# Kernel optimization log

Measured on AMD Instinct MI355X. Metric: run time of the kernel, lower is better.

## Reference

```python
import jax, jax.numpy as jnp
import numpy as np

N = 20000      # nodes
E = 640000     # edges (avg degree 32)
F = 128        # hidden_channels == num_filters
RBF = 64       # num_rbf
H = 8          # num_heads
DH = F // H    # head dim
T = 5          # number of distinct element types present in z
CUT = 5.0      # cutoff_upper (cutoff_lower = 0)


def setup_inputs() -> dict:
    key = jax.random.key(0)
    ks = jax.random.split(key, 20)
    s = 0.05
    inp = {
        "x": jax.random.normal(ks[0], (N, F), jnp.float32),
        "z": jax.random.randint(ks[1], (N,), 0, T, jnp.int32),
        "edge_index": jax.random.randint(ks[2], (2, E), 0, N, jnp.int32),
        "edge_weight": jax.random.uniform(ks[3], (E,), jnp.float32) * CUT,
        "edge_attr": jax.random.normal(ks[4], (E, RBF), jnp.float32),
        # ElemConv params
        "lin1_w": jax.random.normal(ks[5], (F, F), jnp.float32) / np.sqrt(F),
        "f_w1": jax.random.normal(ks[6], (F, RBF), jnp.float32) / np.sqrt(RBF),
        "f_b1": jnp.zeros((F,), jnp.float32),
        "f_w2": jax.random.normal(ks[7], (F, F), jnp.float32) / np.sqrt(F),
        "f_b2": jnp.zeros((F,), jnp.float32),
        # ElemAttn params
        "q_w": jax.random.normal(ks[8], (F, F), jnp.float32) / np.sqrt(F),
        "q_b": jax.random.normal(ks[9], (F,), jnp.float32) * s,
        "k_w": jax.random.normal(ks[10], (F, F), jnp.float32) / np.sqrt(F),
        "k_b": jax.random.normal(ks[11], (F,), jnp.float32) * s,
        "v_w": jax.random.normal(ks[12], (F, F), jnp.float32) / np.sqrt(F),
        "v_b": jax.random.normal(ks[13], (F,), jnp.float32) * s,
        "o1_w": jax.random.normal(ks[14], (F, F), jnp.float32) / np.sqrt(F),
        "o1_b": jax.random.normal(ks[15], (F,), jnp.float32) * s,
        "o2_w": jax.random.normal(ks[16], (F, F), jnp.float32) / np.sqrt(F),
        "o2_b": jax.random.normal(ks[17], (F,), jnp.float32) * s,
    }
    return inp


def reference(x, z, edge_index, edge_weight, edge_attr,
              lin1_w, f_w1, f_b1, f_w2, f_b2,
              q_w, q_b, k_w, k_b, v_w, v_b, o1_w, o1_b, o2_w, o2_b):
    silu = jax.nn.silu
    src, dst = edge_index[0], edge_index[1]

    # ---- ElemConv ----
    # CosineCutoff (cutoff_lower = 0)
    C = 0.5 * (jnp.cos(edge_weight * (jnp.pi / CUT)) + 1.0)
    C = C * (edge_weight < CUT).astype(x.dtype)
    # filter_net(edge_attr) * C
    W = silu(edge_attr @ f_w1.T + f_b1) @ f_w2.T + f_b2          # [E, F]
    W = W * C[:, None]
    xl = x @ lin1_w.T                                             # [N, F]
    msg = xl[src] * W                                             # [E, F]
    # aggregate by unique (z_j, dst) pair == dense [N, T] slot grid
    seg = dst * T + z[src]                                        # [E]
    y = jax.ops.segment_sum(msg, seg, num_segments=N * T).reshape(N, T, F)
    cnt = jax.ops.segment_sum(jnp.ones((E,), x.dtype), seg, num_segments=N * T)
    pm = (cnt > 0).astype(x.dtype).reshape(N, T)                  # presence mask

    # ---- ElemAttn (block-diagonal per target node over present slots) ----
    q = (y @ q_w.T + q_b).reshape(N, T, H, DH)
    k = (y @ k_w.T + k_b).reshape(N, T, H, DH)
    v = (y @ v_w.T + v_b).reshape(N, T, H, DH)
    attn = silu(jnp.einsum('nihd,njhd->nhij', q, k))              # [N, H, T, T]
    attn = attn * (pm[:, None, :, None] * pm[:, None, None, :])
    out = jnp.einsum('nhij,njhd->nihd', attn, v).reshape(N, T, F)
    out = out @ o1_w.T + o1_b                                     # [N, T, F]
    node = jnp.einsum('ntf,nt->nf', out, pm)                      # scatter-add by node
    return silu(node @ o2_w.T + o2_b)                             # [N, F]
```

## Files before the change

### kernel.cpp

```cpp
#include <hip/hip_runtime.h>

#define N_NODES 20000
#define E_EDGES 640000
#define F_DIM 128
#define RBF_DIM 64
#define T_TYPES 5
#define NSEG (N_NODES * T_TYPES)
#define EPB 128

typedef __attribute__((ext_vector_type(8))) short short8;
typedef __attribute__((ext_vector_type(4))) float f32x4;

__device__ __forceinline__ float silu_f(float x) { return x / (1.0f + __expf(-x)); }

__device__ __forceinline__ ushort f2bf(float f) {
  unsigned u = __float_as_uint(f);
  u += 0x7fffu + ((u >> 16) & 1u);
  return (ushort)(u >> 16);
}
__device__ __forceinline__ float bf2f(ushort u) {
  return __uint_as_float(((unsigned)u) << 16);
}
__device__ __forceinline__ unsigned cvt_pk(float lo, float hi) {
  unsigned r;
  asm("v_cvt_pk_bf16_f32 %0, %1, %2" : "=v"(r) : "v"(lo), "v"(hi));
  return r;
}
union S8U4 {
  short8 s;
  unsigned u[4];
};

__global__ __launch_bounds__(256) void prep_kernel(
    const float* __restrict__ w1, const float* __restrict__ w2,
    const float* __restrict__ qw, const float* __restrict__ kw,
    const float* __restrict__ vw, ushort* __restrict__ w1b,
    ushort* __restrict__ w2b, ushort* __restrict__ qwb,
    ushort* __restrict__ kwb, ushort* __restrict__ vwb) {
  int i = blockIdx.x * 256 + threadIdx.x;
  if (i < F_DIM * RBF_DIM) w1b[i] = f2bf(w1[i]);
  if (i < F_DIM * F_DIM) {
    w2b[i] = f2bf(w2[i]);
    qwb[i] = f2bf(qw[i]);
    kwb[i] = f2bf(kw[i]);
    vwb[i] = f2bf(vw[i]);
  }
}

__global__ __launch_bounds__(256) void hist_kernel(const int* __restrict__ srcp,
                                                   const int* __restrict__ dstp,
                                                   const int* __restrict__ z,
                                                   int* __restrict__ hist) {
  int e = blockIdx.x * 256 + threadIdx.x;
  int s = srcp[e];
  int seg = dstp[e] * T_TYPES + z[s];
  atomicAdd(&hist[seg], 1);
}

__global__ __launch_bounds__(256) void scan1_kernel(const int* __restrict__ hist,
                                                    int* __restrict__ offs,
                                                    int* __restrict__ bsums) {
  __shared__ int lds[256];
  int tid = threadIdx.x;
  int base = blockIdx.x * 1024 + tid * 4;
  int v[4];
  int s = 0;
#pragma unroll
  for (int i = 0; i < 4; ++i) {
    v[i] = (base + i < NSEG) ? hist[base + i] : 0;
    s += v[i];
  }
  lds[tid] = s;
  __syncthreads();
  for (int d = 1; d < 256; d <<= 1) {
    int t = (tid >= d) ? lds[tid - d] : 0;
    __syncthreads();
    lds[tid] += t;
    __syncthreads();
  }
  int excl = lds[tid] - s;
#pragma unroll
  for (int i = 0; i < 4; ++i) {
    if (base + i < NSEG) offs[base + i] = excl;
    excl += v[i];
  }
  if (tid == 255) bsums[blockIdx.x] = lds[255];
}

__global__ __launch_bounds__(128) void scan2_kernel(int* __restrict__ bsums,
                                                    int nb) {
  __shared__ int lds[128];
  int tid = threadIdx.x;
  int v = (tid < nb) ? bsums[tid] : 0;
  lds[tid] = v;
  __syncthreads();
  for (int d = 1; d < 128; d <<= 1) {
    int t = (tid >= d) ? lds[tid - d] : 0;
    __syncthreads();
    lds[tid] += t;
    __syncthreads();
  }
  if (tid < nb) bsums[tid] = lds[tid] - v;
}

__global__ __launch_bounds__(256) void scan3_kernel(const int* __restrict__ offs,
                                                    const int* __restrict__ bsums,
                                                    int* __restrict__ cursor) {
  int tid = threadIdx.x;
  int base = blockIdx.x * 1024 + tid * 4;
  int add = bsums[blockIdx.x];
#pragma unroll
  for (int i = 0; i < 4; ++i)
    if (base + i < NSEG) cursor[base + i] = offs[base + i] + add;
}

__global__ __launch_bounds__(256) void scatter_kernel(const int* __restrict__ srcp,
                                                      const int* __restrict__ dstp,
                                                      const int* __restrict__ z,
                                                      int* __restrict__ cursor,
                                                      int* __restrict__ perm) {
  int e = blockIdx.x * 256 + threadIdx.x;
  int s = srcp[e];
  int seg = dstp[e] * T_TYPES + z[s];
  int pos = atomicAdd(&cursor[seg], 1);
  perm[pos] = e;
}

__global__ __launch_bounds__(128) void lin1_kernel(const float* __restrict__ x,
                                                   const float* __restrict__ w,
                                                   ushort* __restrict__ xlb) {
  __shared__ float xs[8 * 128];
  int tid = threadIdx.x;
  int n0 = blockIdx.x * 8;
  const float4* xg = (const float4*)(x + (size_t)n0 * 128);
  float4* xs4 = (float4*)xs;
  for (int i = tid; i < 256; i += 128) xs4[i] = xg[i];
  __syncthreads();
  int f = tid;
  float acc[8] = {};
  const float4* w4 = (const float4*)(w + (size_t)f * 128);
  for (int j4 = 0; j4 < 32; ++j4) {
    float4 wv = w4[j4];
#pragma unroll
    for (int n = 0; n < 8; ++n) {
      float4 xv = xs4[n * 32 + j4];
      acc[n] += wv.x * xv.x + wv.y * xv.y + wv.z * xv.z + wv.w * xv.w;
    }
  }
  for (int n = 0; n < 8; ++n) xlb[(size_t)(n0 + n) * 128 + f] = f2bf(acc[n]);
}

__global__ __launch_bounds__(256, 4) void edge_mfma_kernel(
    const float* __restrict__ edge_attr, const int* __restrict__ srcp,
    const int* __restrict__ dstp, const float* __restrict__ ewp,
    const int* __restrict__ z, const int* __restrict__ perm,
    const ushort* __restrict__ w1b, const float* __restrict__ b1,
    const ushort* __restrict__ w2b, const float* __restrict__ b2,
    const ushort* __restrict__ xlb, float* __restrict__ y) {
  __shared__ ushort hs[128 * 136];
  __shared__ float sC[EPB];
  __shared__ int srcoff[EPB];
  __shared__ int sseg[EPB];
  __shared__ float sb1[128];
  __shared__ float sb2[128];
  __shared__ unsigned long long smask[2];

  const int tid = threadIdx.x;
  const int e0 = blockIdx.x * EPB;
  const int lane = tid & 63;
  const int w = tid >> 6;
  const int wm = w >> 1, wn = w & 1;
  const int lr = lane & 15, lh = lane >> 4;

  int prow[4];
#pragma unroll
  for (int fm = 0; fm < 4; ++fm) prow[fm] = perm[e0 + wm * 64 + fm * 16 + lr];

  if (tid < EPB) {
    int e = perm[e0 + tid];
    int s = srcp[e];
    srcoff[tid] = s * 128;
    sseg[tid] = dstp[e] * T_TYPES + z[s];
    float wd = ewp[e];
    float c = 0.5f * (__cosf(wd * 0.6283185307179586f) + 1.0f);
    sC[tid] = (wd < 5.0f) ? c : 0.0f;
    sb1[tid] = b1[tid];
    sb2[tid] = b2[tid];
  }

  f32x4 acc[4][4] = {};
#pragma unroll
  for (int ks = 0; ks < 2; ++ks) {
    const int k0 = ks * 32;
    short8 af[4], bfr[4];
#pragma unroll
    for (int fm = 0; fm < 4; ++fm) {
      const float* ap = edge_attr + (size_t)prow[fm] * 64 + k0 + lh * 8;
      float4 a0 = *(const float4*)ap;
      float4 a1 = *(const float4*)(ap + 4);
      S8U4 t;
      t.u[0] = cvt_pk(a0.x, a0.y);
      t.u[1] = cvt_pk(a0.z, a0.w);
      t.u[2] = cvt_pk(a1.x, a1.y);
      t.u[3] = cvt_pk(a1.z, a1.w);
      af[fm] = t.s;
    }
#pragma unroll
    for (int fc = 0; fc < 4; ++fc)
      bfr[fc] = *(const short8*)(w1b + (size_t)(wn * 64 + fc * 16 + lr) * 64 +
                                 k0 + lh * 8);
#pragma unroll
    for (int fm = 0; fm < 4; ++fm)
#pragma unroll
      for (int fc = 0; fc < 4; ++fc)
        acc[fm][fc] = __builtin_amdgcn_mfma_f32_16x16x32_bf16(
            af[fm], bfr[fc], acc[fm][fc], 0, 0, 0);
  }
  __syncthreads();

  if (tid < EPB) {
    int head = (tid == 0) || (sseg[tid] != sseg[tid - 1]);
    unsigned long long m = __ballot(head);
    if ((tid & 63) == 0) smask[tid >> 6] = m;
  }

#pragma unroll
  for (int fm = 0; fm < 4; ++fm) {
#pragma unroll
    for (int fc = 0; fc < 4; ++fc) {
#pragma unroll
      for (int rp = 0; rp < 4; rp += 2) {
        int ml0 = wm * 64 + fm * 16 + lh * 4 + rp;
        int ml1 = ml0 + 1;
        int n = wn * 64 + fc * 16 + lr;
        float h0 = silu_f(acc[fm][fc][rp] + sb1[n]);
        float h1 = silu_f(acc[fm][fc][rp + 1] + sb1[n]);
        unsigned u = cvt_pk(h0, h1);
        hs[(ml0 * 256 + ((n * 2) ^ ((ml0 & 7) << 4))) >> 1] = (ushort)u;
        hs[(ml1 * 256 + ((n * 2) ^ ((ml1 & 7) << 4))) >> 1] = (ushort)(u >> 16);
      }
    }
  }
  __syncthreads();

  f32x4 acc2[4][4] = {};
#pragma unroll
  for (int ks = 0; ks < 4; ++ks) {
    const int k0 = ks * 32;
    short8 af[4], bfr[4];
#pragma unroll
    for (int fm = 0; fm < 4; ++fm) {
      int ml = wm * 64 + fm * 16 + lr;
      int byte_in_row = (k0 * 2 + lh * 16) ^ ((ml & 7) << 4);
      af[fm] = *(const short8*)&hs[(ml * 256 + byte_in_row) >> 1];
    }
#pragma unroll
    for (int fc = 0; fc < 4; ++fc)
      bfr[fc] = *(const short8*)(w2b + (size_t)(wn * 64 + fc * 16 + lr) * 128 +
                                 k0 + lh * 8);
#pragma unroll
    for (int fm = 0; fm < 4; ++fm)
#pragma unroll
      for (int fc = 0; fc < 4; ++fc)
        acc2[fm][fc] = __builtin_amdgcn_mfma_f32_16x16x32_bf16(
            af[fm], bfr[fc], acc2[fm][fc], 0, 0, 0);
  }
  __syncthreads();

#pragma unroll
  for (int fm = 0; fm < 4; ++fm) {
#pragma unroll
    for (int rp = 0; rp < 4; rp += 2) {
      int ml0 = wm * 64 + fm * 16 + lh * 4 + rp;
      float c0 = sC[ml0], c1 = sC[ml0 + 1];
#pragma unroll
      for (int fc = 0; fc < 4; ++fc) {
        int n = wn * 64 + fc * 16 + lr;
        float v0 = (acc2[fm][fc][rp] + sb2[n]) * c0;
        float v1 = (acc2[fm][fc][rp + 1] + sb2[n]) * c1;
        *(unsigned*)&hs[n * 136 + ml0] = cvt_pk(v0, v1);
      }
    }
  }
  __syncthreads();

  {
    int col = tid & 127;
    int q = tid >> 7;
    int rbase = q * 64;
    unsigned long long m = smask[q];
    float acc3 = 0.0f;
    int cur = sseg[rbase];
#pragma unroll
    for (int it = 0; it < 8; ++it) {
      int r0 = rbase + it * 8;
      short8 mv = *(const short8*)&hs[col * 136 + r0];
      ushort xv[8];
#pragma unroll
      for (int j = 0; j < 8; ++j) xv[j] = xlb[(size_t)srcoff[r0 + j] + col];
#pragma unroll
      for (int j = 0; j < 8; ++j) {
        if ((it | j) && ((m >> (it * 8 + j)) & 1ull)) {
          atomicAdd(&y[(size_t)cur * 128 + col], acc3);
          acc3 = 0.0f;
          cur = sseg[r0 + j];
        }
        acc3 += bf2f((ushort)mv[j]) * bf2f(xv[j]);
      }
    }
    atomicAdd(&y[(size_t)cur * 128 + col], acc3);
  }
}

#define QS 136
#define NB 16
__global__ __launch_bounds__(256) void attn_fused_kernel(
    const float* __restrict__ y, const int* __restrict__ hist,
    const ushort* __restrict__ qwb, const ushort* __restrict__ kwb,
    const ushort* __restrict__ vwb, const float* __restrict__ qb,
    const float* __restrict__ kb, const float* __restrict__ vb,
    float* __restrict__ sout) {
  __shared__ ushort qs[80 * QS];
  __shared__ ushort ks_[80 * QS];
  __shared__ ushort vs[80 * QS];
  __shared__ float aa[NB * 8 * 5];
  __shared__ float pmv[80];
  __shared__ float sxb[3][128];

  const int tid = threadIdx.x;
  const int n0 = blockIdx.x * NB;
  const int row0 = n0 * T_TYPES;
  const int lane = tid & 63;
  const int w = tid >> 6;
  const int lr = lane & 15, lh = lane >> 4;

  if (tid < 128) {
    sxb[0][tid] = qb[tid];
    sxb[1][tid] = kb[tid];
    sxb[2][tid] = vb[tid];
  }
  if (tid < 80) pmv[tid] = (hist[(size_t)row0 + tid] > 0) ? 1.0f : 0.0f;

  short8 A[4][5];
#pragma unroll
  for (int ksi = 0; ksi < 4; ++ksi) {
#pragma unroll
    for (int fm = 0; fm < 5; ++fm) {
      const float* ap =
          y + (size_t)(row0 + fm * 16 + lr) * 128 + ksi * 32 + lh * 8;
      float4 a0 = *(const float4*)ap;
      float4 a1 = *(const float4*)(ap + 4);
      S8U4 t;
      t.u[0] = cvt_pk(a0.x, a0.y);
      t.u[1] = cvt_pk(a0.z, a0.w);
      t.u[2] = cvt_pk(a1.x, a1.y);
      t.u[3] = cvt_pk(a1.z, a1.w);
      A[ksi][fm] = t.s;
    }
  }
  __syncthreads();

  const ushort* Wp[3] = {qwb, kwb, vwb};
  ushort* Xp[3] = {qs, ks_, vs};
#pragma unroll
  for (int m = 0; m < 3; ++m) {
    f32x4 acc[5][2] = {};
#pragma unroll
    for (int ksi = 0; ksi < 4; ++ksi) {
      short8 B[2];
#pragma unroll
      for (int fc = 0; fc < 2; ++fc)
        B[fc] = *(const short8*)(Wp[m] + (size_t)(w * 32 + fc * 16 + lr) * 128 +
                                 ksi * 32 + lh * 8);
#pragma unroll
      for (int fm = 0; fm < 5; ++fm)
#pragma unroll
        for (int fc = 0; fc < 2; ++fc)
          acc[fm][fc] = __builtin_amdgcn_mfma_f32_16x16x32_bf16(
              A[ksi][fm], B[fc], acc[fm][fc], 0, 0, 0);
    }
#pragma unroll
    for (int fm = 0; fm < 5; ++fm)
#pragma unroll
      for (int fc = 0; fc < 2; ++fc)
#pragma unroll
        for (int rp = 0; rp < 4; rp += 2) {
          int rrow = fm * 16 + lh * 4 + rp;
          int col = w * 32 + fc * 16 + lr;
          float v0 = acc[fm][fc][rp] + sxb[m][col];
          float v1 = acc[fm][fc][rp + 1] + sxb[m][col];
          unsigned u = cvt_pk(v0, v1);
          Xp[m][rrow * QS + col] = (ushort)u;
          Xp[m][(rrow + 1) * QS + col] = (ushort)(u >> 16);
        }
  }
  __syncthreads();

  if (tid < NB * 8) {
    int n = tid >> 3, h = tid & 7;
    float kv[5][16];
#pragma unroll
    for (int j = 0; j < 5; ++j) {
      short8 v0 = *(const short8*)&ks_[(n * 5 + j) * QS + h * 16];
      short8 v1 = *(const short8*)&ks_[(n * 5 + j) * QS + h * 16 + 8];
#pragma unroll
      for (int d = 0; d < 8; ++d) {
        kv[j][d] = bf2f((ushort)v0[d]);
        kv[j][d + 8] = bf2f((ushort)v1[d]);
      }
    }
    float a[5] = {};
    for (int i = 0; i < 5; ++i) {
      float qv[16];
      short8 q0 = *(const short8*)&qs[(n * 5 + i) * QS + h * 16];
      short8 q1 = *(const short8*)&qs[(n * 5 + i) * QS + h * 16 + 8];
#pragma unroll
      for (int d = 0; d < 8; ++d) {
        qv[d] = bf2f((ushort)q0[d]);
        qv[d + 8] = bf2f((ushort)q1[d]);
      }
      float pmi = pmv[n * 5 + i];
#pragma unroll
      for (int j = 0; j < 5; ++j) {
        float dd = 0.0f;
#pragma unroll
        for (int d = 0; d < 16; ++d) dd += qv[d] * kv[j][d];
        a[j] += pmi * silu_f(dd);
      }
    }
#pragma unroll
    for (int j = 0; j < 5; ++j) aa[(n * 8 + h) * 5 + j] = a[j] * pmv[n * 5 + j];
  }
  __syncthreads();

  {
    int n = tid >> 4;
    int o = tid & 15;
    int f0 = o * 8;
    int h = f0 >> 4;
    float acc8[8] = {};
#pragma unroll
    for (int j = 0; j < 5; ++j) {
      float a = aa[(n * 8 + h) * 5 + j];
      short8 vv8 = *(const short8*)&vs[(n * 5 + j) * QS + f0];
#pragma unroll
      for (int d = 0; d < 8; ++d) acc8[d] += a * bf2f((ushort)vv8[d]);
    }
    float* op = sout + (size_t)(n0 + n) * 128 + f0;
    *(float4*)op = make_float4(acc8[0], acc8[1], acc8[2], acc8[3]);
    *(float4*)(op + 4) = make_float4(acc8[4], acc8[5], acc8[6], acc8[7]);
  }
}

__global__ __launch_bounds__(128) void out_kernel(
    const float* __restrict__ sbufg, const int* __restrict__ hist,
    const float* __restrict__ o1w, const float* __restrict__ o1b,
    const float* __restrict__ o2w, const float* __restrict__ o2b,
    float* __restrict__ outp) {
  __shared__ float sb[8 * 128];
  __shared__ float t1[8 * 128];
  __shared__ float npm[8];
  int tid = threadIdx.x;
  int n0 = blockIdx.x * 8;
  const float4* sg4 = (const float4*)(sbufg + (size_t)n0 * 128);
  float4* sb4 = (float4*)sb;
  for (int i = tid; i < 256; i += 128) sb4[i] = sg4[i];
  if (tid < 8) {
    float s = 0.0f;
    for (int t = 0; t < T_TYPES; ++t)
      s += (hist[(size_t)(n0 + tid) * T_TYPES + t] > 0) ? 1.0f : 0.0f;
    npm[tid] = s;
  }
  __syncthreads();
  int f = tid;
  {
    const float4* wg = (const float4*)(o1w + (size_t)f * 128);
    float acc[8] = {};
    for (int j4 = 0; j4 < 32; ++j4) {
      float4 wv = wg[j4];
#pragma unroll
      for (int n = 0; n < 8; ++n) {
        float4 sv = sb4[n * 32 + j4];
        acc[n] += wv.x * sv.x + wv.y * sv.y + wv.z * sv.z + wv.w * sv.w;
      }
    }
    float bb = o1b[f];
    for (int n = 0; n < 8; ++n) t1[n * 128 + f] = acc[n] + npm[n] * bb;
  }
  __syncthreads();
  {
    const float4* wg = (const float4*)(o2w + (size_t)f * 128);
    const float4* t14 = (const float4*)t1;
    float acc[8] = {};
    for (int j4 = 0; j4 < 32; ++j4) {
      float4 wv = wg[j4];
#pragma unroll
      for (int n = 0; n < 8; ++n) {
        float4 tv = t14[n * 32 + j4];
        acc[n] += wv.x * tv.x + wv.y * tv.y + wv.z * tv.z + wv.w * tv.w;
      }
    }
    float bb = o2b[f];
    for (int n = 0; n < 8; ++n) outp[(size_t)(n0 + n) * 128 + f] = silu_f(acc[n] + bb);
  }
}

extern "C" void kernel_launch(void* const* d_in, const int* in_sizes, int n_in,
                              void* d_out, int out_size, void* d_ws, size_t ws_size,
                              hipStream_t stream) {
  const float* x = (const float*)d_in[0];
  const int* z = (const int*)d_in[1];
  const int* ei = (const int*)d_in[2];
  const float* ew = (const float*)d_in[3];
  const float* ea = (const float*)d_in[4];
  const float* lin1_w = (const float*)d_in[5];
  const float* fw1 = (const float*)d_in[6];
  const float* fb1 = (const float*)d_in[7];
  const float* fw2 = (const float*)d_in[8];
  const float* fb2 = (const float*)d_in[9];
  const float* qw = (const float*)d_in[10];
  const float* qb = (const float*)d_in[11];
  const float* kw = (const float*)d_in[12];
  const float* kb = (const float*)d_in[13];
  const float* vw = (const float*)d_in[14];
  const float* vb = (const float*)d_in[15];
  const float* o1w = (const float*)d_in[16];
  const float* o1b = (const float*)d_in[17];
  const float* o2w = (const float*)d_in[18];
  const float* o2b = (const float*)d_in[19];
  float* outp = (float*)d_out;
  float* ws = (float*)d_ws;

  float* sbuf = ws;
  float* y = sbuf + (size_t)N_NODES * F_DIM;
  ushort* xlb = (ushort*)(y + (size_t)NSEG * F_DIM);
  ushort* w1b = xlb + (size_t)N_NODES * F_DIM;
  ushort* w2b = w1b + F_DIM * RBF_DIM;
  ushort* qwb = w2b + F_DIM * F_DIM;
  ushort* kwb = qwb + F_DIM * F_DIM;
  ushort* vwb = kwb + F_DIM * F_DIM;
  int* hist = (int*)(vwb + F_DIM * F_DIM);
  int* offs = hist + NSEG;
  int* cursor = offs + NSEG;
  int* bsums = cursor + NSEG;
  int* perm = bsums + 128;

  const int* srcp = ei;
  const int* dstp = ei + E_EDGES;
  const int NB_SCAN = (NSEG + 1023) / 1024;

  hipMemsetAsync(y, 0, (size_t)NSEG * F_DIM * sizeof(float), stream);
  hipMemsetAsync(hist, 0, (size_t)NSEG * sizeof(int), stream);

  prep_kernel<<<64, 256, 0, stream>>>(fw1, fw2, qw, kw, vw, w1b, w2b, qwb, kwb, vwb);
  hist_kernel<<<E_EDGES / 256, 256, 0, stream>>>(srcp, dstp, z, hist);
  scan1_kernel<<<NB_SCAN, 256, 0, stream>>>(hist, offs, bsums);
  scan2_kernel<<<1, 128, 0, stream>>>(bsums, NB_SCAN);
  scan3_kernel<<<NB_SCAN, 256, 0, stream>>>(offs, bsums, cursor);
  scatter_kernel<<<E_EDGES / 256, 256, 0, stream>>>(srcp, dstp, z, cursor, perm);
  lin1_kernel<<<N_NODES / 8, 128, 0, stream>>>(x, lin1_w, xlb);
  edge_mfma_kernel<<<E_EDGES / EPB, 256, 0, stream>>>(ea, srcp, dstp, ew, z, perm,
                                                      w1b, fb1, w2b, fb2, xlb, y);
  attn_fused_kernel<<<N_NODES / NB, 256, 0, stream>>>(y, hist, qwb, kwb, vwb, qb,
                                                      kb, vb, sbuf);
  out_kernel<<<N_NODES / 8, 128, 0, stream>>>(sbuf, hist, o1w, o1b, o2w, o2b, outp);
}
```

Before: 362.6 us.

## Cut edge-kernel atomics and syncs, and shrink attention LDS to two buffers

The edge kernel now keeps the bias values in registers and folds the SiLU write of the hidden tile into the first stage, which removes one block barrier. Its scatter phase now has each thread handle two adjacent columns over 32 rows. Segments that start and end inside that 32-row chunk are written with plain stores instead of atomics, which relies on the y buffer being zeroed and on edges being sorted by segment. The attention kernel drops one of its three LDS staging buffers by computing the V projection into the Q buffer after the scores are done. This lowers shared memory per block to allow higher occupancy, at the cost of one extra barrier and serialized projection work.

```diff
diff --git a/kernel.cpp b/kernel.cpp
--- a/kernel.cpp
+++ b/kernel.cpp
@@ -161,8 +161,6 @@
   __shared__ float sC[EPB];
   __shared__ int srcoff[EPB];
   __shared__ int sseg[EPB];
-  __shared__ float sb1[128];
-  __shared__ float sb2[128];
   __shared__ unsigned long long smask[2];
 
   const int tid = threadIdx.x;
@@ -175,6 +173,14 @@
   int prow[4];
 #pragma unroll
   for (int fm = 0; fm < 4; ++fm) prow[fm] = perm[e0 + wm * 64 + fm * 16 + lr];
+
+  float rb1[4], rb2[4];
+#pragma unroll
+  for (int fc = 0; fc < 4; ++fc) {
+    int n = wn * 64 + fc * 16 + lr;
+    rb1[fc] = b1[n];
+    rb2[fc] = b2[n];
+  }
 
   if (tid < EPB) {
     int e = perm[e0 + tid];
@@ -184,8 +190,6 @@
     float wd = ewp[e];
     float c = 0.5f * (__cosf(wd * 0.6283185307179586f) + 1.0f);
     sC[tid] = (wd < 5.0f) ? c : 0.0f;
-    sb1[tid] = b1[tid];
-    sb2[tid] = b2[tid];
   }
 
   f32x4 acc[4][4] = {};
@@ -216,6 +220,24 @@
         acc[fm][fc] = __builtin_amdgcn_mfma_f32_16x16x32_bf16(
             af[fm], bfr[fc], acc[fm][fc], 0, 0, 0);
   }
+
+#pragma unroll
+  for (int fm = 0; fm < 4; ++fm) {
+#pragma unroll
+    for (int fc = 0; fc < 4; ++fc) {
+#pragma unroll
+      for (int rp = 0; rp < 4; rp += 2) {
+        int ml0 = wm * 64 + fm * 16 + lh * 4 + rp;
+        int ml1 = ml0 + 1;
+        int n = wn * 64 + fc * 16 + lr;
+        float h0 = silu_f(acc[fm][fc][rp] + rb1[fc]);
+        float h1 = silu_f(acc[fm][fc][rp + 1] + rb1[fc]);
+        unsigned u = cvt_pk(h0, h1);
+        hs[(ml0 * 256 + ((n * 2) ^ ((ml0 & 7) << 4))) >> 1] = (ushort)u;
+        hs[(ml1 * 256 + ((n * 2) ^ ((ml1 & 7) << 4))) >> 1] = (ushort)(u >> 16);
+      }
+    }
+  }
   __syncthreads();
 
   if (tid < EPB) {
@@ -224,25 +246,6 @@
     if ((tid & 63) == 0) smask[tid >> 6] = m;
   }
 
-#pragma unroll
-  for (int fm = 0; fm < 4; ++fm) {
-#pragma unroll
-    for (int fc = 0; fc < 4; ++fc) {
-#pragma unroll
-      for (int rp = 0; rp < 4; rp += 2) {
-        int ml0 = wm * 64 + fm * 16 + lh * 4 + rp;
-        int ml1 = ml0 + 1;
-        int n = wn * 64 + fc * 16 + lr;
-        float h0 = silu_f(acc[fm][fc][rp] + sb1[n]);
-        float h1 = silu_f(acc[fm][fc][rp + 1] + sb1[n]);
-        unsigned u = cvt_pk(h0, h1);
-        hs[(ml0 * 256 + ((n * 2) ^ ((ml0 & 7) << 4))) >> 1] = (ushort)u;
-        hs[(ml1 * 256 + ((n * 2) ^ ((ml1 & 7) << 4))) >> 1] = (ushort)(u >> 16);
-      }
-    }
-  }
-  __syncthreads();
-
   f32x4 acc2[4][4] = {};
 #pragma unroll
   for (int ks = 0; ks < 4; ++ks) {
@@ -276,8 +279,8 @@
 #pragma unroll
       for (int fc = 0; fc < 4; ++fc) {
         int n = wn * 64 + fc * 16 + lr;
-        float v0 = (acc2[fm][fc][rp] + sb2[n]) * c0;
-        float v1 = (acc2[fm][fc][rp + 1] + sb2[n]) * c1;
+        float v0 = (acc2[fm][fc][rp] + rb2[fc]) * c0;
+        float v1 = (acc2[fm][fc][rp + 1] + rb2[fc]) * c1;
         *(unsigned*)&hs[n * 136 + ml0] = cvt_pk(v0, v1);
       }
     }
@@ -285,30 +288,46 @@
   __syncthreads();
 
   {
-    int col = tid & 127;
-    int q = tid >> 7;
-    int rbase = q * 64;
-    unsigned long long m = smask[q];
-    float acc3 = 0.0f;
+    int cp = tid & 63;
+    int q = tid >> 6;
+    int rbase = q * 32;
+    int c0 = cp * 2;
+    unsigned mm = (unsigned)(smask[q >> 1] >> ((q & 1) * 32));
+    float a0 = 0.0f, a1 = 0.0f;
     int cur = sseg[rbase];
-#pragma unroll
-    for (int it = 0; it < 8; ++it) {
+    bool first = true;
+#pragma unroll
+    for (int it = 0; it < 4; ++it) {
       int r0 = rbase + it * 8;
-      short8 mv = *(const short8*)&hs[col * 136 + r0];
-      ushort xv[8];
-#pragma unroll
-      for (int j = 0; j < 8; ++j) xv[j] = xlb[(size_t)srcoff[r0 + j] + col];
+      short8 m0 = *(const short8*)&hs[c0 * 136 + r0];
+      short8 m1 = *(const short8*)&hs[(c0 + 1) * 136 + r0];
+      unsigned xv[8];
+#pragma unroll
+      for (int j = 0; j < 8; ++j)
+        xv[j] = *(const unsigned*)&xlb[(size_t)srcoff[r0 + j] + c0];
 #pragma unroll
       for (int j = 0; j < 8; ++j) {
-        if ((it | j) && ((m >> (it * 8 + j)) & 1ull)) {
-          atomicAdd(&y[(size_t)cur * 128 + col], acc3);
-          acc3 = 0.0f;
+        int rr = it * 8 + j;
+        if (rr && ((mm >> rr) & 1u)) {
+          float* yp = &y[(size_t)cur * 128 + c0];
+          if (first) {
+            atomicAdd(yp, a0);
+            atomicAdd(yp + 1, a1);
+            first = false;
+          } else {
+            yp[0] = a0;
+            yp[1] = a1;
+          }
+          a0 = a1 = 0.0f;
           cur = sseg[r0 + j];
         }
-        acc3 += bf2f((ushort)mv[j]) * bf2f(xv[j]);
-      }
-    }
-    atomicAdd(&y[(size_t)cur * 128 + col], acc3);
+        a0 += bf2f((ushort)m0[j]) * bf2f((ushort)xv[j]);
+        a1 += bf2f((ushort)m1[j]) * bf2f((ushort)(xv[j] >> 16));
+      }
+    }
+    float* yp = &y[(size_t)cur * 128 + c0];
+    atomicAdd(yp, a0);
+    atomicAdd(yp + 1, a1);
   }
 }
 
@@ -320,9 +339,8 @@
     const ushort* __restrict__ vwb, const float* __restrict__ qb,
     const float* __restrict__ kb, const float* __restrict__ vb,
     float* __restrict__ sout) {
-  __shared__ ushort qs[80 * QS];
-  __shared__ ushort ks_[80 * QS];
-  __shared__ ushort vs[80 * QS];
+  __shared__ ushort bufA[80 * QS];
+  __shared__ ushort bufB[80 * QS];
   __shared__ float aa[NB * 8 * 5];
   __shared__ float pmv[80];
   __shared__ float sxb[3][128];
@@ -360,17 +378,15 @@
   }
   __syncthreads();
 
-  const ushort* Wp[3] = {qwb, kwb, vwb};
-  ushort* Xp[3] = {qs, ks_, vs};
-#pragma unroll
-  for (int m = 0; m < 3; ++m) {
+  auto do_proj = [&](const ushort* __restrict__ Wb, const float* bias_row,
+                     ushort* __restrict__ dst) {
     f32x4 acc[5][2] = {};
 #pragma unroll
     for (int ksi = 0; ksi < 4; ++ksi) {
       short8 B[2];
 #pragma unroll
       for (int fc = 0; fc < 2; ++fc)
-        B[fc] = *(const short8*)(Wp[m] + (size_t)(w * 32 + fc * 16 + lr) * 128 +
+        B[fc] = *(const short8*)(Wb + (size_t)(w * 32 + fc * 16 + lr) * 128 +
                                  ksi * 32 + lh * 8);
 #pragma unroll
       for (int fm = 0; fm < 5; ++fm)
@@ -387,13 +403,16 @@
         for (int rp = 0; rp < 4; rp += 2) {
           int rrow = fm * 16 + lh * 4 + rp;
           int col = w * 32 + fc * 16 + lr;
-          float v0 = acc[fm][fc][rp] + sxb[m][col];
-          float v1 = acc[fm][fc][rp + 1] + sxb[m][col];
+          float v0 = acc[fm][fc][rp] + bias_row[col];
+          float v1 = acc[fm][fc][rp + 1] + bias_row[col];
           unsigned u = cvt_pk(v0, v1);
-          Xp[m][rrow * QS + col] = (ushort)u;
-          Xp[m][(rrow + 1) * QS + col] = (ushort)(u >> 16);
+          dst[rrow * QS + col] = (ushort)u;
+          dst[(rrow + 1) * QS + col] = (ushort)(u >> 16);
         }
-  }
+  };
+
+  do_proj(qwb, sxb[0], bufA);
+  do_proj(kwb, sxb[1], bufB);
   __syncthreads();
 
   if (tid < NB * 8) {
@@ -401,8 +420,8 @@
     float kv[5][16];
 #pragma unroll
     for (int j = 0; j < 5; ++j) {
-      short8 v0 = *(const short8*)&ks_[(n * 5 + j) * QS + h * 16];
-      short8 v1 = *(const short8*)&ks_[(n * 5 + j) * QS + h * 16 + 8];
+      short8 v0 = *(const short8*)&bufB[(n * 5 + j) * QS + h * 16];
+      short8 v1 = *(const short8*)&bufB[(n * 5 + j) * QS + h * 16 + 8];
 #pragma unroll
       for (int d = 0; d < 8; ++d) {
         kv[j][d] = bf2f((ushort)v0[d]);
@@ -412,8 +431,8 @@
     float a[5] = {};
     for (int i = 0; i < 5; ++i) {
       float qv[16];
-      short8 q0 = *(const short8*)&qs[(n * 5 + i) * QS + h * 16];
-      short8 q1 = *(const short8*)&qs[(n * 5 + i) * QS + h * 16 + 8];
+      short8 q0 = *(const short8*)&bufA[(n * 5 + i) * QS + h * 16];
+      short8 q1 = *(const short8*)&bufA[(n * 5 + i) * QS + h * 16 + 8];
 #pragma unroll
       for (int d = 0; d < 8; ++d) {
         qv[d] = bf2f((ushort)q0[d]);
@@ -431,6 +450,9 @@
 #pragma unroll
     for (int j = 0; j < 5; ++j) aa[(n * 8 + h) * 5 + j] = a[j] * pmv[n * 5 + j];
   }
+  __syncthreads();
+
+  do_proj(vwb, sxb[2], bufA);
   __syncthreads();
 
   {
@@ -442,7 +464,7 @@
 #pragma unroll
     for (int j = 0; j < 5; ++j) {
       float a = aa[(n * 8 + h) * 5 + j];
-      short8 vv8 = *(const short8*)&vs[(n * 5 + j) * QS + f0];
+      short8 vv8 = *(const short8*)&bufA[(n * 5 + j) * QS + f0];
 #pragma unroll
       for (int d = 0; d < 8; ++d) acc8[d] += a * bf2f((ushort)vv8[d]);
     }
```

Result: no change. 359.1 us (-1.0%).
